# Performance work log

Measured on AMD Instinct MI355X. Metric: run time of the kernel, lower is better.

The kernel has to match this reference:

```python
import jax, jax.numpy as jnp
import numpy as np

B, N, D, H, KD, VD, O = 64, 2048, 256, 8, 32, 32, 256
LARGE = 1e9
EPS = 1e-10


def setup_inputs() -> dict:
    key = jax.random.key(0)
    ks = jax.random.split(key, 8)
    return {
        "q_data": jax.random.normal(ks[0], (B, N, D), dtype=jnp.float32),
        "m_data": jax.random.normal(ks[1], (B, N, D), dtype=jnp.float32),
        "q_mask": jnp.ones((B, N, 1), dtype=jnp.float32),
        "query_w": jax.random.normal(ks[2], (D, H, KD), dtype=jnp.float32) * 0.05,
        "key_w": jax.random.normal(ks[3], (D, KD), dtype=jnp.float32) * 0.05,
        "value_w": jax.random.normal(ks[4], (D, VD), dtype=jnp.float32) * 0.05,
        "gating_w": jax.random.normal(ks[5], (D, H, VD), dtype=jnp.float32) * 0.05,
        "gating_b": jnp.ones((H, VD), dtype=jnp.float32),
        "output_w": jax.random.normal(ks[6], (H, VD, O), dtype=jnp.float32) * 0.05,
        "output_b": jnp.zeros((O,), dtype=jnp.float32),
    }


def reference(q_data, m_data, q_mask, query_w, key_w, value_w, gating_w, gating_b, output_w, output_b):
    key_dim = query_w.shape[-1]
    # values/keys are shared across heads: [B, N, KD/VD]
    v = jnp.einsum('bka,ac->bkc', m_data, value_w)
    # masked mean over the query axis -> single query per batch element
    q_avg = jnp.sum(q_mask * q_data, axis=1) / (jnp.sum(q_mask, axis=1) + EPS)  # [B, D]
    q = jnp.einsum('ba,ahc->bhc', q_avg, query_w) * (key_dim ** -0.5)  # [B, H, KD]
    k = jnp.einsum('bka,ac->bkc', m_data, key_w)  # [B, N, KD]
    bias = LARGE * (q_mask[:, None, :, 0] - 1.0)  # [B, 1, N]
    logits = jnp.einsum('bhc,bkc->bhk', q, k) + bias  # [B, H, N]
    weights = jax.nn.softmax(logits, axis=-1)
    weighted_avg = jnp.einsum('bhk,bkc->bhc', weights, v)  # [B, H, VD]
    gate = jax.nn.sigmoid(jnp.einsum('bqc,chv->bqhv', q_data, gating_w) + gating_b)  # [B, N, H, VD]
    gated = weighted_avg[:, None] * gate  # broadcast single attn result over queries
    return jnp.einsum('bqhc,hco->bqo', gated, output_w) + output_b  # [B, N, O]
```

## Files before the change

kernel.cpp:

```cpp
#include <hip/hip_runtime.h>

#define B_ 64
#define N_ 2048
#define D_ 256
#define H_ 8
#define LARGE_ 1e9f
#define EPS_ 1e-10f

typedef __attribute__((ext_vector_type(4))) float f32x4;
typedef __attribute__((ext_vector_type(8))) short s16x8;

#define WS_QKBF 0
#define WS_WGP  524288
#define WS_QPART 655360
#define WS_MPART 1179648
#define WS_MX   1181696
#define WS_SM   1247232
#define WS_WA   1312768
#define WS_WMP  1378304
#define WS_WPP  1378304

__device__ __forceinline__ unsigned short f2bf(float f) {
  union { float f; unsigned u; } v; v.f = f;
  unsigned r = v.u + 0x7fffu + ((v.u >> 16) & 1u);
  return (unsigned short)(r >> 16);
}
__device__ __forceinline__ float bf2f(unsigned short s) {
  union { unsigned u; float f; } v; v.u = ((unsigned)s) << 16;
  return v.f;
}

__global__ void kA(const float* __restrict__ q_data, const float* __restrict__ q_mask,
                   const float* __restrict__ gating_w, float* __restrict__ qpart,
                   float* __restrict__ mpart, unsigned short* __restrict__ wgp) {
  int blk = blockIdx.x, t = threadIdx.x;
  if (blk < 512) {
    int b = blk >> 3, n0 = (blk & 7) * 256;
    __shared__ float msk[256];
    __shared__ float qred[4][256];
    __shared__ float mred[4];
    msk[t] = q_mask[b * N_ + n0 + t];
    __syncthreads();
    int w = t >> 6, d4 = t & 63;
    const float* qbase = q_data + ((size_t)(b * N_ + n0)) * D_;
    f32x4 acc = {0.f, 0.f, 0.f, 0.f};
    #pragma unroll 4
    for (int i = 0; i < 64; ++i) {
      int r = i * 4 + w;
      f32x4 v = *(const f32x4*)(qbase + (size_t)r * D_ + d4 * 4);
      float mk = msk[r];
      acc += v * mk;
    }
    *(f32x4*)(&qred[w][d4 * 4]) = acc;
    float mv = msk[t];
    for (int off = 32; off; off >>= 1) mv += __shfl_xor(mv, off);
    if ((t & 63) == 0) mred[t >> 6] = mv;
    __syncthreads();
    qpart[((size_t)blk) * 256 + t] = qred[0][t] + qred[1][t] + qred[2][t] + qred[3][t];
    if (t == 0) mpart[blk] = mred[0] + mred[1] + mred[2] + mred[3];
  } else {
    int base = (blk - 512) * 1024;
    for (int i = 0; i < 4; ++i) {
      int a = base + i * 256 + t;
      int sc = a >> 9, l = (a >> 3) & 63, j = a & 7;
      int s = sc >> 4, c = sc & 15, lh = l >> 4, ll = l & 15;
      int k = s * 32 + lh * 8 + j, n = c * 16 + ll;
      wgp[a] = f2bf(gating_w[k * 256 + n]);
    }
  }
}

__global__ void kB(const float* __restrict__ qpart, const float* __restrict__ mpart,
                   const float* __restrict__ query_w, const float* __restrict__ key_w,
                   unsigned short* __restrict__ qkbf) {
  int b = blockIdx.x, t = threadIdx.x;
  __shared__ float qa[256];
  __shared__ float ql[256];
  float s = 0.f;
  #pragma unroll
  for (int p = 0; p < 8; ++p) s += qpart[((size_t)(b * 8 + p)) * 256 + t];
  float ms = 0.f;
  #pragma unroll
  for (int p = 0; p < 8; ++p) ms += mpart[b * 8 + p];
  qa[t] = s / (ms + EPS_);
  __syncthreads();
  float acc = 0.f;
  #pragma unroll 4
  for (int a = 0; a < 256; ++a) acc += qa[a] * query_w[a * 256 + t];
  ql[t] = acc * 0.17677669529663687f;
  __syncthreads();
  float v8[8];
  #pragma unroll
  for (int h = 0; h < 8; ++h) {
    float v = 0.f;
    #pragma unroll
    for (int c = 0; c < 32; ++c) v += key_w[t * 32 + c] * ql[h * 32 + c];
    v8[h] = v;
  }
  int si = t >> 5, lh = (t >> 3) & 3, j = t & 7;
  unsigned short* base = qkbf + ((size_t)(b * 8 + si) * 64) * 8;
  #pragma unroll
  for (int h = 0; h < 8; ++h) {
    base[(lh * 16 + h) * 8 + j] = f2bf(v8[h]);
    base[(lh * 16 + 8 + h) * 8 + j] = 0;
  }
}

__global__ void kM(const float* __restrict__ m_data, const float* __restrict__ q_mask,
                   const unsigned short* __restrict__ qkbf, unsigned short* __restrict__ wm_part,
                   float* __restrict__ mx_part, float* __restrict__ sm_part) {
  int b = blockIdx.y, ch = blockIdx.x, n0 = ch * 64, t = threadIdx.x;
  __shared__ __align__(16) unsigned char sM[64 * 528];
  __shared__ f32x4 pW[64][2];
  __shared__ float red[4][8];
  __shared__ float hval[8];
  {
    int w = t >> 6, d4 = t & 63;
    #pragma unroll
    for (int i = 0; i < 16; ++i) {
      int r = i * 4 + w;
      f32x4 v = *(const f32x4*)(m_data + ((size_t)(b * N_ + n0 + r)) * D_ + d4 * 4);
      uint2 pp;
      pp.x = f2bf(v[0]) | ((unsigned)f2bf(v[1]) << 16);
      pp.y = f2bf(v[2]) | ((unsigned)f2bf(v[3]) << 16);
      *(uint2*)(sM + r * 528 + d4 * 8) = pp;
    }
  }
  __syncthreads();
  int lane = t & 63, w = t >> 6;
  int l15 = lane & 15, lhi = lane >> 4;
  const s16x8* A = (const s16x8*)qkbf + (size_t)b * 512;
  s16x8 areg[8];
  #pragma unroll
  for (int s = 0; s < 8; ++s) areg[s] = A[s * 64 + lane];
  f32x4 acc = {0.f, 0.f, 0.f, 0.f};
  int nrow = w * 16 + l15;
  #pragma unroll
  for (int s = 0; s < 8; ++s) {
    s16x8 bfr = *(const s16x8*)(sM + nrow * 528 + s * 64 + lhi * 16);
    acc = __builtin_amdgcn_mfma_f32_16x16x32_bf16(areg[s], bfr, acc, 0, 0, 0);
  }
  float bias = LARGE_ * (q_mask[b * N_ + n0 + nrow] - 1.f);
  float lg[4];
  #pragma unroll
  for (int r = 0; r < 4; ++r) lg[r] = (lhi < 2) ? (acc[r] + bias) : -3.4e38f;
  #pragma unroll
  for (int off = 8; off; off >>= 1)
    #pragma unroll
    for (int r = 0; r < 4; ++r) lg[r] = fmaxf(lg[r], __shfl_xor(lg[r], off));
  if (l15 == 0 && lhi < 2)
    #pragma unroll
    for (int r = 0; r < 4; ++r) red[w][lhi * 4 + r] = lg[r];
  __syncthreads();
  if (t < 8) {
    float m = fmaxf(fmaxf(red[0][t], red[1][t]), fmaxf(red[2][t], red[3][t]));
    hval[t] = m;
    mx_part[((size_t)(b * 32 + ch)) * 8 + t] = m;
  }
  __syncthreads();
  float pv[4], ps[4];
  #pragma unroll
  for (int r = 0; r < 4; ++r) {
    float M = hval[(lhi & 1) * 4 + r];
    float e = __expf(acc[r] + bias - M);
    pv[r] = e;
    ps[r] = (lhi < 2) ? e : 0.f;
  }
  if (lhi < 2) {
    f32x4 pq = {pv[0], pv[1], pv[2], pv[3]};
    pW[nrow][lhi] = pq;
  }
  #pragma unroll
  for (int off = 8; off; off >>= 1)
    #pragma unroll
    for (int r = 0; r < 4; ++r) ps[r] += __shfl_xor(ps[r], off);
  if (l15 == 0 && lhi < 2)
    #pragma unroll
    for (int r = 0; r < 4; ++r) red[w][lhi * 4 + r] = ps[r];
  __syncthreads();
  if (t < 8)
    sm_part[((size_t)(b * 32 + ch)) * 8 + t] = red[0][t] + red[1][t] + red[2][t] + red[3][t];
  f32x4 vacc[8];
  #pragma unroll
  for (int h = 0; h < 8; ++h) vacc[h] = (f32x4){0.f, 0.f, 0.f, 0.f};
  #pragma unroll 4
  for (int i = 0; i < 16; ++i) {
    int r = w * 16 + i;
    uint2 pp = *(const uint2*)(sM + r * 528 + lane * 8);
    f32x4 mv;
    mv[0] = bf2f(pp.x & 0xffff); mv[1] = bf2f(pp.x >> 16);
    mv[2] = bf2f(pp.y & 0xffff); mv[3] = bf2f(pp.y >> 16);
    f32x4 w0 = pW[r][0], w1 = pW[r][1];
    vacc[0] += mv * w0[0]; vacc[1] += mv * w0[1]; vacc[2] += mv * w0[2]; vacc[3] += mv * w0[3];
    vacc[4] += mv * w1[0]; vacc[5] += mv * w1[1]; vacc[6] += mv * w1[2]; vacc[7] += mv * w1[3];
  }
  __syncthreads();
  float* red2 = (float*)sM;
  #pragma unroll
  for (int h = 0; h < 8; ++h) *(f32x4*)(&red2[(w * 8 + h) * 256 + lane * 4]) = vacc[h];
  __syncthreads();
  float s8[8];
  #pragma unroll
  for (int h = 0; h < 8; ++h)
    s8[h] = red2[h * 256 + t] + red2[(8 + h) * 256 + t] + red2[(16 + h) * 256 + t] +
            red2[(24 + h) * 256 + t];
  uint4 u;
  u.x = f2bf(s8[0]) | ((unsigned)f2bf(s8[1]) << 16);
  u.y = f2bf(s8[2]) | ((unsigned)f2bf(s8[3]) << 16);
  u.z = f2bf(s8[4]) | ((unsigned)f2bf(s8[5]) << 16);
  u.w = f2bf(s8[6]) | ((unsigned)f2bf(s8[7]) << 16);
  *(uint4*)(wm_part + ((size_t)((b * 32 + ch) * 256 + t)) * 8) = u;
}

__global__ void kFX(const unsigned short* __restrict__ wm_part, const float* __restrict__ mx_part,
                    const float* __restrict__ sm_part, const float* __restrict__ value_w,
                    const float* __restrict__ output_w, unsigned short* __restrict__ wpp) {
  int b = blockIdx.x, t = threadIdx.x;
  __shared__ float s_mx[256], s_sm[256], scl[256];
  __shared__ float gmx[8], gden[8];
  __shared__ float wml[8][256];
  __shared__ float sOW[32 * 260];
  __shared__ float wa[256];
  s_mx[t] = mx_part[(size_t)b * 256 + t];
  s_sm[t] = sm_part[(size_t)b * 256 + t];
  __syncthreads();
  if (t < 8) {
    float m = -3.4e38f;
    for (int c = 0; c < 32; ++c) m = fmaxf(m, s_mx[c * 8 + t]);
    gmx[t] = m;
  }
  __syncthreads();
  scl[t] = __expf(s_mx[t] - gmx[t & 7]);
  __syncthreads();
  if (t < 8) {
    float d = 0.f;
    for (int c = 0; c < 32; ++c) d += s_sm[c * 8 + t] * scl[c * 8 + t];
    gden[t] = d;
  }
  float acc[8] = {0.f, 0.f, 0.f, 0.f, 0.f, 0.f, 0.f, 0.f};
  for (int c = 0; c < 32; ++c) {
    uint4 u = *(const uint4*)(wm_part + ((size_t)((b * 32 + c) * 256 + t)) * 8);
    const float* sc = &scl[c * 8];
    acc[0] += bf2f(u.x & 0xffff) * sc[0]; acc[1] += bf2f(u.x >> 16) * sc[1];
    acc[2] += bf2f(u.y & 0xffff) * sc[2]; acc[3] += bf2f(u.y >> 16) * sc[3];
    acc[4] += bf2f(u.z & 0xffff) * sc[4]; acc[5] += bf2f(u.z >> 16) * sc[5];
    acc[6] += bf2f(u.w & 0xffff) * sc[6]; acc[7] += bf2f(u.w >> 16) * sc[7];
  }
  #pragma unroll
  for (int h = 0; h < 8; ++h) wml[h][t] = acc[h];
  __syncthreads();
  {
    int h = t >> 5, v = t & 31;
    float s = 0.f;
    #pragma unroll 4
    for (int d = 0; d < 256; ++d) s += wml[h][d] * value_w[d * 32 + v];
    wa[t] = s / gden[h];
  }
  unsigned short* wp = wpp + (size_t)b * 65536;
  for (int sb = 0; sb < 8; ++sb) {
    __syncthreads();
    const f32x4* src = (const f32x4*)(output_w + sb * 32 * 256);
    #pragma unroll
    for (int i = 0; i < 8; ++i) {
      int idx4 = i * 256 + t;
      f32x4 v = src[idx4];
      int rr = idx4 >> 6, c4 = idx4 & 63;
      *(f32x4*)(&sOW[rr * 260 + c4 * 4]) = v;
    }
    __syncthreads();
    int abase = sb * 8192;
    for (int it = 0; it < 32; ++it) {
      int a = abase + it * 256 + t;
      int l = (a >> 3) & 63, j = a & 7;
      int c = (a >> 9) & 15, lh = l >> 4, ll = l & 15;
      int hvl = lh * 8 + j, o = c * 16 + ll;
      wp[a] = f2bf(wa[sb * 32 + hvl] * sOW[hvl * 260 + o]);
    }
  }
}

__global__ void __launch_bounds__(256, 4) kG(
    const float* __restrict__ q_data, const float* __restrict__ gating_b,
    const float* __restrict__ output_b, const unsigned short* __restrict__ wgp,
    const unsigned short* __restrict__ wpp, float* __restrict__ out) {
  int b = blockIdx.y, row0 = blockIdx.x * 64, t = threadIdx.x;
  __shared__ __align__(16) unsigned char sG[64 * 528];
  {
    int w = t >> 6, d4 = t & 63;
    #pragma unroll
    for (int i = 0; i < 16; ++i) {
      int r = i * 4 + w;
      f32x4 v = *(const f32x4*)(q_data + ((size_t)(b * N_ + row0 + r)) * D_ + d4 * 4);
      uint2 pp;
      pp.x = f2bf(v[0]) | ((unsigned)f2bf(v[1]) << 16);
      pp.y = f2bf(v[2]) | ((unsigned)f2bf(v[3]) << 16);
      *(uint2*)(sG + r * 528 + d4 * 8) = pp;
    }
  }
  __syncthreads();
  int lane = t & 63, cg = t >> 6;
  int l15 = lane & 15, lhi = lane >> 4;
  const f32x4 z = {0.f, 0.f, 0.f, 0.f};
  f32x4 acc[16];
  #pragma unroll
  for (int f = 0; f < 16; ++f) acc[f] = z;
  const s16x8* Bg = (const s16x8*)wgp;
  #pragma unroll
  for (int s = 0; s < 8; ++s) {
    s16x8 af[4], bfr[4];
    #pragma unroll
    for (int rt = 0; rt < 4; ++rt)
      af[rt] = *(const s16x8*)(sG + (rt * 16 + l15) * 528 + s * 64 + lhi * 16);
    #pragma unroll
    for (int ct = 0; ct < 4; ++ct) bfr[ct] = Bg[(s * 16 + cg * 4 + ct) * 64 + lane];
    #pragma unroll
    for (int rt = 0; rt < 4; ++rt)
      #pragma unroll
      for (int ct = 0; ct < 4; ++ct)
        acc[rt * 4 + ct] =
            __builtin_amdgcn_mfma_f32_16x16x32_bf16(af[rt], bfr[ct], acc[rt * 4 + ct], 0, 0, 0);
  }
  __syncthreads();
  {
    float gb[4];
    #pragma unroll
    for (int ct = 0; ct < 4; ++ct) gb[ct] = gating_b[cg * 64 + ct * 16 + l15];
    #pragma unroll
    for (int rt = 0; rt < 4; ++rt)
      #pragma unroll
      for (int ct = 0; ct < 4; ++ct) {
        int col = cg * 64 + ct * 16 + l15;
        #pragma unroll
        for (int r = 0; r < 4; ++r) {
          float x = acc[rt * 4 + ct][r] + gb[ct];
          float g = 1.f / (1.f + __expf(-x));
          int row = rt * 16 + lhi * 4 + r;
          *(unsigned short*)(sG + row * 528 + col * 2) = f2bf(g);
        }
      }
  }
  __syncthreads();
  #pragma unroll
  for (int f = 0; f < 16; ++f) acc[f] = z;
  const s16x8* Bp = (const s16x8*)wpp + (size_t)b * 8192;
  #pragma unroll
  for (int s = 0; s < 8; ++s) {
    s16x8 af[4], bfr[4];
    #pragma unroll
    for (int rt = 0; rt < 4; ++rt)
      af[rt] = *(const s16x8*)(sG + (rt * 16 + l15) * 528 + s * 64 + lhi * 16);
    #pragma unroll
    for (int ct = 0; ct < 4; ++ct) bfr[ct] = Bp[(s * 16 + cg * 4 + ct) * 64 + lane];
    #pragma unroll
    for (int rt = 0; rt < 4; ++rt)
      #pragma unroll
      for (int ct = 0; ct < 4; ++ct)
        acc[rt * 4 + ct] =
            __builtin_amdgcn_mfma_f32_16x16x32_bf16(af[rt], bfr[ct], acc[rt * 4 + ct], 0, 0, 0);
  }
  __syncthreads();
  float* fOut = (float*)sG;
  float ob[4];
  #pragma unroll
  for (int ct = 0; ct < 4; ++ct) ob[ct] = output_b[cg * 64 + ct * 16 + l15];
  #pragma unroll
  for (int p = 0; p < 2; ++p) {
    #pragma unroll
    for (int rt2 = 0; rt2 < 2; ++rt2) {
      int rt = p * 2 + rt2;
      #pragma unroll
      for (int ct = 0; ct < 4; ++ct) {
        int col = cg * 64 + ct * 16 + l15;
        #pragma unroll
        for (int r = 0; r < 4; ++r)
          fOut[(rt2 * 16 + lhi * 4 + r) * 260 + col] = acc[rt * 4 + ct][r] + ob[ct];
      }
    }
    __syncthreads();
    {
      int w = t >> 6, c4 = t & 63;
      #pragma unroll
      for (int j = 0; j < 8; ++j) {
        int r32 = j * 4 + w;
        f32x4 v = *(const f32x4*)(fOut + r32 * 260 + c4 * 4);
        *(f32x4*)(out + ((size_t)(b * N_ + row0 + p * 32 + r32)) * D_ + c4 * 4) = v;
      }
    }
    __syncthreads();
  }
}

extern "C" void kernel_launch(void* const* d_in, const int* in_sizes, int n_in,
                              void* d_out, int out_size, void* d_ws, size_t ws_size,
                              hipStream_t stream) {
  const float* q_data   = (const float*)d_in[0];
  const float* m_data   = (const float*)d_in[1];
  const float* q_mask   = (const float*)d_in[2];
  const float* query_w  = (const float*)d_in[3];
  const float* key_w    = (const float*)d_in[4];
  const float* value_w  = (const float*)d_in[5];
  const float* gating_w = (const float*)d_in[6];
  const float* gating_b = (const float*)d_in[7];
  const float* output_w = (const float*)d_in[8];
  const float* output_b = (const float*)d_in[9];
  float* out = (float*)d_out;
  char* ws = (char*)d_ws;

  unsigned short* qkbf = (unsigned short*)(ws + WS_QKBF);
  unsigned short* wgp  = (unsigned short*)(ws + WS_WGP);
  float* qpart = (float*)(ws + WS_QPART);
  float* mpart = (float*)(ws + WS_MPART);
  float* mx    = (float*)(ws + WS_MX);
  float* sm    = (float*)(ws + WS_SM);
  unsigned short* wmp = (unsigned short*)(ws + WS_WMP);
  unsigned short* wpp = (unsigned short*)(ws + WS_WPP);

  kA<<<576, 256, 0, stream>>>(q_data, q_mask, gating_w, qpart, mpart, wgp);
  kB<<<64, 256, 0, stream>>>(qpart, mpart, query_w, key_w, qkbf);
  kM<<<dim3(32, 64), 256, 0, stream>>>(m_data, q_mask, qkbf, wmp, mx, sm);
  kFX<<<64, 256, 0, stream>>>(wmp, mx, sm, value_w, output_w, wpp);
  kG<<<dim3(32, 64), 256, 0, stream>>>(q_data, gating_b, output_b, wgp, wpp, out);
}
```

Before: 486.3 us.

## Split q-mean reduction into more blocks and split output-weight prep kernel

New measurement: 474.5 us. 2.4% less time.

```diff
diff --git a/kernel.cpp b/kernel.cpp
--- a/kernel.cpp
+++ b/kernel.cpp
@@ -13,12 +13,12 @@
 #define WS_QKBF 0
 #define WS_WGP  524288
 #define WS_QPART 655360
-#define WS_MPART 1179648
-#define WS_MX   1181696
-#define WS_SM   1247232
-#define WS_WA   1312768
-#define WS_WMP  1378304
-#define WS_WPP  1378304
+#define WS_MPART 2752512
+#define WS_MX   2760704
+#define WS_SM   2826240
+#define WS_WA   2891776
+#define WS_WMP  2957312
+#define WS_WPP  2957312
 
 __device__ __forceinline__ unsigned short f2bf(float f) {
   union { float f; unsigned u; } v; v.f = f;
@@ -34,32 +34,31 @@
                    const float* __restrict__ gating_w, float* __restrict__ qpart,
                    float* __restrict__ mpart, unsigned short* __restrict__ wgp) {
   int blk = blockIdx.x, t = threadIdx.x;
-  if (blk < 512) {
-    int b = blk >> 3, n0 = (blk & 7) * 256;
-    __shared__ float msk[256];
+  if (blk < 2048) {
+    int b = blk >> 5, n0 = (blk & 31) * 64;
+    __shared__ float msk[64];
     __shared__ float qred[4][256];
-    __shared__ float mred[4];
-    msk[t] = q_mask[b * N_ + n0 + t];
+    if (t < 64) msk[t] = q_mask[b * N_ + n0 + t];
     __syncthreads();
     int w = t >> 6, d4 = t & 63;
     const float* qbase = q_data + ((size_t)(b * N_ + n0)) * D_;
     f32x4 acc = {0.f, 0.f, 0.f, 0.f};
     #pragma unroll 4
-    for (int i = 0; i < 64; ++i) {
+    for (int i = 0; i < 16; ++i) {
       int r = i * 4 + w;
       f32x4 v = *(const f32x4*)(qbase + (size_t)r * D_ + d4 * 4);
-      float mk = msk[r];
-      acc += v * mk;
+      acc += v * msk[r];
     }
     *(f32x4*)(&qred[w][d4 * 4]) = acc;
-    float mv = msk[t];
-    for (int off = 32; off; off >>= 1) mv += __shfl_xor(mv, off);
-    if ((t & 63) == 0) mred[t >> 6] = mv;
     __syncthreads();
     qpart[((size_t)blk) * 256 + t] = qred[0][t] + qred[1][t] + qred[2][t] + qred[3][t];
-    if (t == 0) mpart[blk] = mred[0] + mred[1] + mred[2] + mred[3];
+    if (t < 64) {
+      float mv = msk[t];
+      for (int off = 32; off; off >>= 1) mv += __shfl_xor(mv, off);
+      if (t == 0) mpart[blk] = mv;
+    }
   } else {
-    int base = (blk - 512) * 1024;
+    int base = (blk - 2048) * 1024;
     for (int i = 0; i < 4; ++i) {
       int a = base + i * 256 + t;
       int sc = a >> 9, l = (a >> 3) & 63, j = a & 7;
@@ -78,10 +77,10 @@
   __shared__ float ql[256];
   float s = 0.f;
   #pragma unroll
-  for (int p = 0; p < 8; ++p) s += qpart[((size_t)(b * 8 + p)) * 256 + t];
+  for (int p = 0; p < 32; ++p) s += qpart[((size_t)(b * 32 + p)) * 256 + t];
   float ms = 0.f;
   #pragma unroll
-  for (int p = 0; p < 8; ++p) ms += mpart[b * 8 + p];
+  for (int p = 0; p < 32; ++p) ms += mpart[b * 32 + p];
   qa[t] = s / (ms + EPS_);
   __syncthreads();
   float acc = 0.f;
@@ -212,15 +211,13 @@
   *(uint4*)(wm_part + ((size_t)((b * 32 + ch) * 256 + t)) * 8) = u;
 }
 
-__global__ void kFX(const unsigned short* __restrict__ wm_part, const float* __restrict__ mx_part,
+__global__ void kF1(const unsigned short* __restrict__ wm_part, const float* __restrict__ mx_part,
                     const float* __restrict__ sm_part, const float* __restrict__ value_w,
-                    const float* __restrict__ output_w, unsigned short* __restrict__ wpp) {
+                    float* __restrict__ wa_g) {
   int b = blockIdx.x, t = threadIdx.x;
   __shared__ float s_mx[256], s_sm[256], scl[256];
   __shared__ float gmx[8], gden[8];
   __shared__ float wml[8][256];
-  __shared__ float sOW[32 * 260];
-  __shared__ float wa[256];
   s_mx[t] = mx_part[(size_t)b * 256 + t];
   s_sm[t] = sm_part[(size_t)b * 256 + t];
   __syncthreads();
@@ -249,17 +246,25 @@
   #pragma unroll
   for (int h = 0; h < 8; ++h) wml[h][t] = acc[h];
   __syncthreads();
-  {
-    int h = t >> 5, v = t & 31;
-    float s = 0.f;
-    #pragma unroll 4
-    for (int d = 0; d < 256; ++d) s += wml[h][d] * value_w[d * 32 + v];
-    wa[t] = s / gden[h];
-  }
+  int h = t >> 5, v = t & 31;
+  float s = 0.f;
+  #pragma unroll 4
+  for (int d = 0; d < 256; ++d) s += wml[h][d] * value_w[d * 32 + v];
+  wa_g[b * 256 + t] = s / gden[h];
+}
+
+__global__ void kF2(const float* __restrict__ wa_g, const float* __restrict__ output_w,
+                    unsigned short* __restrict__ wpp) {
+  int blk = blockIdx.x, t = threadIdx.x;
+  int b = blk >> 2, quad = blk & 3;
+  __shared__ float sOW[32 * 260];
+  __shared__ float wa[256];
+  wa[t] = wa_g[b * 256 + t];
   unsigned short* wp = wpp + (size_t)b * 65536;
-  for (int sb = 0; sb < 8; ++sb) {
-    __syncthreads();
-    const f32x4* src = (const f32x4*)(output_w + sb * 32 * 256);
+  for (int half = 0; half < 2; ++half) {
+    int srow = quad * 64 + half * 32;
+    __syncthreads();
+    const f32x4* src = (const f32x4*)(output_w + srow * 256);
     #pragma unroll
     for (int i = 0; i < 8; ++i) {
       int idx4 = i * 256 + t;
@@ -268,13 +273,13 @@
       *(f32x4*)(&sOW[rr * 260 + c4 * 4]) = v;
     }
     __syncthreads();
-    int abase = sb * 8192;
+    int abase = quad * 16384 + half * 8192;
     for (int it = 0; it < 32; ++it) {
       int a = abase + it * 256 + t;
       int l = (a >> 3) & 63, j = a & 7;
       int c = (a >> 9) & 15, lh = l >> 4, ll = l & 15;
       int hvl = lh * 8 + j, o = c * 16 + ll;
-      wp[a] = f2bf(wa[sb * 32 + hvl] * sOW[hvl * 260 + o]);
+      wp[a] = f2bf(wa[srow + hvl] * sOW[hvl * 260 + o]);
     }
   }
 }
@@ -412,12 +417,14 @@
   float* mpart = (float*)(ws + WS_MPART);
   float* mx    = (float*)(ws + WS_MX);
   float* sm    = (float*)(ws + WS_SM);
+  float* wa    = (float*)(ws + WS_WA);
   unsigned short* wmp = (unsigned short*)(ws + WS_WMP);
   unsigned short* wpp = (unsigned short*)(ws + WS_WPP);
 
-  kA<<<576, 256, 0, stream>>>(q_data, q_mask, gating_w, qpart, mpart, wgp);
+  kA<<<2112, 256, 0, stream>>>(q_data, q_mask, gating_w, qpart, mpart, wgp);
   kB<<<64, 256, 0, stream>>>(qpart, mpart, query_w, key_w, qkbf);
   kM<<<dim3(32, 64), 256, 0, stream>>>(m_data, q_mask, qkbf, wmp, mx, sm);
-  kFX<<<64, 256, 0, stream>>>(wmp, mx, sm, value_w, output_w, wpp);
+  kF1<<<64, 256, 0, stream>>>(wmp, mx, sm, value_w, wa);
+  kF2<<<256, 256, 0, stream>>>(wa, output_w, wpp);
   kG<<<dim3(32, 64), 256, 0, stream>>>(q_data, gating_b, output_b, wgp, wpp, out);
 }
```
